# Kernel optimization log

Hardware: AMD Instinct MI355X
Metric: run time of the kernel (lower is better)

## Reference

```python
import jax, jax.numpy as jnp
import numpy as np

H = 512  # hidden_dim
IN = 4   # input_dim
OUT = 2  # output_dim
T_OBS = 30
T_PRED = 60
B = 4096


def _gru_cell(x, h, Wih, Whh, bih, bhh):
    # PyTorch GRU cell math. x: (B, D_in), h: (B, H)
    gi = x @ Wih.T + bih          # (B, 3H)
    gh = h @ Whh.T + bhh          # (B, 3H)
    i_r, i_z, i_n = jnp.split(gi, 3, axis=-1)
    h_r, h_z, h_n = jnp.split(gh, 3, axis=-1)
    r = jax.nn.sigmoid(i_r + h_r)
    z = jax.nn.sigmoid(i_z + h_z)
    n = jnp.tanh(i_n + r * h_n)
    return (1.0 - z) * n + z * h


def _gru_layer(xs, h0, Wih, Whh, bih, bhh):
    # xs: (T, B, D_in) -> outputs (T, B, H), final h (B, H)
    def step(h, x):
        h_new = _gru_cell(x, h, Wih, Whh, bih, bhh)
        return h_new, h_new
    h_last, ys = jax.lax.scan(step, h0, xs)
    return ys, h_last


def setup_inputs() -> dict:
    key = jax.random.key(0)
    ks = jax.random.split(key, 16)
    s = 0.05
    inp = {
        "x": jax.random.normal(ks[0], (B, T_OBS, IN), dtype=jnp.float32),
        # encoder layer 0
        "W_ih0": jax.random.normal(ks[1], (3 * H, IN)) * s,
        "W_hh0": jax.random.normal(ks[2], (3 * H, H)) * s,
        "b_ih0": jax.random.normal(ks[3], (3 * H,)) * s,
        "b_hh0": jax.random.normal(ks[4], (3 * H,)) * s,
        # encoder layer 1
        "W_ih1": jax.random.normal(ks[5], (3 * H, H)) * s,
        "W_hh1": jax.random.normal(ks[6], (3 * H, H)) * s,
        "b_ih1": jax.random.normal(ks[7], (3 * H,)) * s,
        "b_hh1": jax.random.normal(ks[8], (3 * H,)) * s,
        # decoder GRU (input_dim = OUT)
        "W_ihd": jax.random.normal(ks[9], (3 * H, OUT)) * s,
        "W_hhd": jax.random.normal(ks[10], (3 * H, H)) * s,
        "b_ihd": jax.random.normal(ks[11], (3 * H,)) * s,
        "b_hhd": jax.random.normal(ks[12], (3 * H,)) * s,
        # output head
        "W_fc": jax.random.normal(ks[13], (OUT, H)) * s,
        "b_fc": jax.random.normal(ks[14], (OUT,)) * s,
    }
    return inp


def reference(x, W_ih0, W_hh0, b_ih0, b_hh0, W_ih1, W_hh1, b_ih1, b_hh1,
              W_ihd, W_hhd, b_ihd, b_hhd, W_fc, b_fc):
    dtype = x.dtype
    xs = jnp.transpose(x, (1, 0, 2))  # (T, B, IN)
    h0 = jnp.zeros((x.shape[0], H), dtype=dtype)
    # 2-layer encoder GRU (dropout=identity at inference)
    ys0, _ = _gru_layer(xs, h0, W_ih0, W_hh0, b_ih0, b_hh0)
    ys1, h_last = _gru_layer(ys0, h0, W_ih1, W_hh1, b_ih1, b_hh1)
    dec_in0 = x[:, -1, :2]  # (B, 2)

    def dec_step(carry, _):
        h, inp = carry
        h_new = _gru_cell(inp, h, W_ihd, W_hhd, b_ihd, b_hhd)
        pred = h_new @ W_fc.T + b_fc  # (B, 2)
        return (h_new, pred), pred

    (_, _), preds = jax.lax.scan(dec_step, (h_last, dec_in0), None, length=T_PRED)
    return jnp.transpose(preds, (1, 0, 2))  # (B, T_PRED, OUT)
```

## Files before the change

kernel.cpp:

```cpp
#include <hip/hip_runtime.h>
#include <math.h>


#define B_SZ  4096
#define H     512
#define TOBS  30
#define TPRED 60

typedef float f32x4 __attribute__((ext_vector_type(4)));
typedef short s16x8 __attribute__((ext_vector_type(8)));
typedef __bf16 bf16x8 __attribute__((ext_vector_type(8)));

__device__ __forceinline__ float b2f(unsigned short u) {
    unsigned v = (unsigned)u << 16; return __builtin_bit_cast(float, v);
}
__device__ __forceinline__ unsigned short f2b(float f) {
    unsigned u = __builtin_bit_cast(unsigned, f);
    return (unsigned short)((u + 0x7FFF + ((u >> 16) & 1)) >> 16);
}

typedef __attribute__((address_space(1))) void gvoid;
typedef __attribute__((address_space(3))) void lvoid;
__device__ __forceinline__ void gl16(const void* g, void* l) {
    __builtin_amdgcn_global_load_lds((gvoid*)g, (lvoid*)l, 16, 0, 0);
}

__device__ __forceinline__ f32x4 mfma_bf16(s16x8 a, s16x8 b, f32x4 c) {
    return __builtin_amdgcn_mfma_f32_16x16x32_bf16(
        __builtin_bit_cast(bf16x8, a), __builtin_bit_cast(bf16x8, b), c, 0, 0, 0);
}

__device__ __forceinline__ float sigmoidf_(float v) { return 1.f / (1.f + expf(-v)); }

template<int NJ, int KTOT, int SPLIT>
__device__ __forceinline__ void gemm_core2(
    const unsigned short* __restrict__ A0, const unsigned short* __restrict__ A1,
    const unsigned short* __restrict__ W,
    int m0, int n0,
    unsigned short* __restrict__ sA, unsigned short* __restrict__ sB,
    f32x4 (&acc)[4][NJ + SPLIT])
{
    const int tid  = threadIdx.x;
    const int lane = tid & 63;
    const int w    = tid >> 6;
    const int wr = w >> 1, wc = w & 1;
    const int lr = lane & 15;
    const int q  = lane >> 4;
    const int wbase = tid & ~63;
    const int NT = KTOT / 64;
    const int ASZ = 128 * 64, BSZ = NJ * 32 * 64;

    auto stage = [&](int buf, int k0) {
        unsigned short* dA = sA + buf * ASZ;
        unsigned short* dB = sB + buf * BSZ;
        const unsigned short* Ab = (SPLIT && k0 >= 512) ? A1 : A0;
        const int ak0 = (SPLIT && k0 >= 512) ? k0 - 512 : k0;
#pragma unroll
        for (int s = 0; s < 4; ++s) {
            int i = s * 256 + tid;
            int row = i >> 3, p = i & 7;
            int c = p ^ (row & 7);
            gl16(Ab + (size_t)(m0 + row) * 512 + ak0 + c * 8, dA + (s * 256 + wbase) * 8);
        }
#pragma unroll
        for (int s = 0; s < NJ; ++s) {
            int i = s * 256 + tid;
            int row = i >> 3, p = i & 7;
            int c = p ^ (row & 7);
            gl16(W + (size_t)(n0 + row) * KTOT + k0 + c * 8, dB + (s * 256 + wbase) * 8);
        }
    };

    stage(0, 0);
    __syncthreads();
#pragma unroll
    for (int ti = 0; ti < NT; ++ti) {
        const int cur = ti & 1;
        if (ti + 1 < NT) stage(cur ^ 1, (ti + 1) * 64);
        const unsigned short* cA = sA + cur * ASZ;
        const unsigned short* cB = sB + cur * BSZ;
#pragma unroll
        for (int kk = 0; kk < 64; kk += 32) {
            int qb = (kk >> 3) + q;
            s16x8 af[4], bf[NJ];
#pragma unroll
            for (int fi = 0; fi < 4; ++fi) {
                int r = wr * 64 + fi * 16 + lr;
                af[fi] = *(const s16x8*)&cA[r * 64 + ((qb ^ (r & 7)) * 8)];
            }
#pragma unroll
            for (int fj = 0; fj < NJ; ++fj) {
                int r = wc * (NJ * 16) + fj * 16 + lr;
                bf[fj] = *(const s16x8*)&cB[r * 64 + ((qb ^ (r & 7)) * 8)];
            }
#pragma unroll
            for (int fi = 0; fi < 4; ++fi)
#pragma unroll
                for (int fj = 0; fj < NJ; ++fj) {
                    const int dst = (SPLIT && fj == NJ - 1 && ti >= NT / 2) ? NJ : fj;
                    acc[fi][dst] = mfma_bf16(af[fi], bf[fj], acc[fi][dst]);
                }
        }
        __syncthreads();
    }
}

__global__ __launch_bounds__(256)
void gemm_enc(const unsigned short* __restrict__ e1_h0, const unsigned short* __restrict__ e1_h1in,
              unsigned short* __restrict__ e1_h1out, const unsigned short* __restrict__ W1,
              const float* __restrict__ bih1, const float* __restrict__ bhh1,
              float* __restrict__ hf1,
              const unsigned short* __restrict__ e0_h0in, unsigned short* __restrict__ e0_h0out,
              const unsigned short* __restrict__ W0,
              const float* __restrict__ x, int t,
              const float* __restrict__ Wih0, const float* __restrict__ bih0,
              const float* __restrict__ bhh0, float* __restrict__ hf0,
              int roles)
{
    __shared__ unsigned short sA[2 * 128 * 64], sB[2 * 96 * 64];

    int bid = (int)blockIdx.x;
    bool isE1;
    if (roles == 3) { isE1 = bid < 512; bid &= 511; }
    else            { isE1 = (roles == 1); }

    int swz = (bid & 7) * 64 + (bid >> 3);
    const int tile_n = swz & 15;
    const int n0 = tile_n * 96;
    const int m0 = (swz >> 4) * 128;

    const int lane = threadIdx.x & 63;
    const int w    = threadIdx.x >> 6;
    const int wrw = w >> 1, wcw = w & 1;
    const int lr = lane & 15, q = lane >> 4;
    const int u = tile_n * 32 + wcw * 16 + lr;

    if (isE1) {
        f32x4 acc[4][4];
#pragma unroll
        for (int i = 0; i < 4; ++i)
#pragma unroll
            for (int j = 0; j < 4; ++j) acc[i][j] = (f32x4){0.f, 0.f, 0.f, 0.f};

        gemm_core2<3, 1024, 1>(e1_h0, e1_h1in, W1, m0, n0, sA, sB, acc);

        float br_ = bih1[u] + bhh1[u];
        float bz_ = bih1[512 + u] + bhh1[512 + u];
        float bni = bih1[1024 + u], bnh = bhh1[1024 + u];
#pragma unroll
        for (int fi = 0; fi < 4; ++fi) {
#pragma unroll
            for (int j = 0; j < 4; ++j) {
                int row = m0 + wrw * 64 + fi * 16 + q * 4 + j;
                float rr = sigmoidf_(acc[fi][0][j] + br_);
                float zz = sigmoidf_(acc[fi][1][j] + bz_);
                float nn = tanhf(acc[fi][2][j] + bni + rr * (acc[fi][3][j] + bnh));
                size_t hidx = (size_t)row * 512 + u;
                float hn = (1.f - zz) * nn + zz * hf1[hidx];
                hf1[hidx] = hn;
                e1_h1out[hidx] = f2b(hn);
            }
        }
    } else {
        f32x4 acc[4][3];
#pragma unroll
        for (int i = 0; i < 4; ++i)
#pragma unroll
            for (int j = 0; j < 3; ++j) acc[i][j] = (f32x4){0.f, 0.f, 0.f, 0.f};

        gemm_core2<3, 512, 0>(e0_h0in, e0_h0in, W0, m0, n0, sA, sB, acc);

        float4 wrv = *(const float4*)(Wih0 + (size_t)u * 4);
        float4 wzv = *(const float4*)(Wih0 + (size_t)(512 + u) * 4);
        float4 wnv = *(const float4*)(Wih0 + (size_t)(1024 + u) * 4);
        float br_ = bih0[u], bz_ = bih0[512 + u], bn_ = bih0[1024 + u];
        float cr_ = bhh0[u], cz_ = bhh0[512 + u], cn_ = bhh0[1024 + u];
#pragma unroll
        for (int fi = 0; fi < 4; ++fi) {
#pragma unroll
            for (int j = 0; j < 4; ++j) {
                int row = m0 + wrw * 64 + fi * 16 + q * 4 + j;
                float4 xv = *(const float4*)(x + (size_t)row * 120 + t * 4);
                float gir = br_ + xv.x * wrv.x + xv.y * wrv.y + xv.z * wrv.z + xv.w * wrv.w;
                float giz = bz_ + xv.x * wzv.x + xv.y * wzv.y + xv.z * wzv.z + xv.w * wzv.w;
                float gin = bn_ + xv.x * wnv.x + xv.y * wnv.y + xv.z * wnv.z + xv.w * wnv.w;
                float rr = sigmoidf_(gir + acc[fi][0][j] + cr_);
                float zz = sigmoidf_(giz + acc[fi][1][j] + cz_);
                float nn = tanhf(gin + rr * (acc[fi][2][j] + cn_));
                size_t hidx = (size_t)row * 512 + u;
                float hn = (1.f - zz) * nn + zz * hf0[hidx];
                hf0[hidx] = hn;
                e0_h0out[hidx] = f2b(hn);
            }
        }
    }
}

__global__ __launch_bounds__(256)
void gemm_d(const unsigned short* __restrict__ A ,
            const unsigned short* __restrict__ W,
            const float* __restrict__ dinbuf, int t,
            const float* __restrict__ Wih, const float* __restrict__ bih,
            const float* __restrict__ bhh, const float* __restrict__ bfc,
            float* __restrict__ hf, unsigned short* __restrict__ hbout,
            float* __restrict__ out)
{
    int bid = (int)blockIdx.x;
    int swz = (bid & 7) * 64 + (bid >> 3);
    const int tile_n = swz & 15;
    const int n0 = tile_n * 128;
    const int m0 = (swz >> 4) * 128;

    __shared__ unsigned short sA[2 * 128 * 64], sB[2 * 128 * 64];
    f32x4 acc[4][4];
#pragma unroll
    for (int i = 0; i < 4; ++i)
#pragma unroll
        for (int j = 0; j < 4; ++j) acc[i][j] = (f32x4){0.f, 0.f, 0.f, 0.f};

    gemm_core2<4, 512, 0>(A, A, W, m0, n0, sA, sB, acc);

    const int lane = threadIdx.x & 63;
    const int w    = threadIdx.x >> 6;
    const int wrw = w >> 1, wcw = w & 1;
    const int lr = lane & 15, q = lane >> 4;
    const int u = tile_n * 32 + wcw * 16 + lr;

    float wr0 = Wih[(size_t)u * 2],          wr1 = Wih[(size_t)u * 2 + 1];
    float wz0 = Wih[(size_t)(512 + u) * 2],  wz1 = Wih[(size_t)(512 + u) * 2 + 1];
    float wn0 = Wih[(size_t)(1024 + u) * 2], wn1 = Wih[(size_t)(1024 + u) * 2 + 1];
    float br_ = bih[u], bz_ = bih[512 + u], bn_ = bih[1024 + u];
    float cr_ = bhh[u], cz_ = bhh[512 + u], cn_ = bhh[1024 + u];
    float bfc0 = bfc[0], bfc1 = bfc[1];
    const bool wout = (tile_n == 0) && (wcw == 0) && (lr == 0);

#pragma unroll
    for (int fi = 0; fi < 4; ++fi) {
#pragma unroll
        for (int j = 0; j < 4; ++j) {
            int row = m0 + wrw * 64 + fi * 16 + q * 4 + j;
            float p0 = __shfl(acc[fi][3][j], (lane & 48) | 0) + bfc0;
            float p1 = __shfl(acc[fi][3][j], (lane & 48) | 1) + bfc1;
            float x0, x1;
            if (t == 0) { x0 = dinbuf[row * 2]; x1 = dinbuf[row * 2 + 1]; }
            else        { x0 = p0; x1 = p1; }
            float gir = br_ + x0 * wr0 + x1 * wr1;
            float giz = bz_ + x0 * wz0 + x1 * wz1;
            float gin = bn_ + x0 * wn0 + x1 * wn1;
            float rr = sigmoidf_(gir + acc[fi][0][j] + cr_);
            float zz = sigmoidf_(giz + acc[fi][1][j] + cz_);
            float nn = tanhf(gin + rr * (acc[fi][2][j] + cn_));
            size_t hidx = (size_t)row * 512 + u;
            float hn = (1.f - zz) * nn + zz * hf[hidx];
            hf[hidx] = hn;
            hbout[hidx] = f2b(hn);
            if (t > 0 && wout) {
                out[(size_t)row * 120 + (t - 1) * 2 + 0] = p0;
                out[(size_t)row * 120 + (t - 1) * 2 + 1] = p1;
            }
        }
    }
}

__global__ __launch_bounds__(64)
void fc_last(const unsigned short* __restrict__ hb, const float* __restrict__ Wfc,
             const float* __restrict__ bfc, float* __restrict__ out)
{
    int row = blockIdx.x, lane = threadIdx.x;
    const unsigned short* hrow = hb + (size_t)row * 512;
    float a0 = 0.f, a1 = 0.f;
#pragma unroll
    for (int kb = 0; kb < 8; ++kb) {
        int k = kb * 64 + lane;
        float hv = b2f(hrow[k]);
        a0 += hv * Wfc[k];
        a1 += hv * Wfc[512 + k];
    }
#pragma unroll
    for (int m = 32; m; m >>= 1) { a0 += __shfl_xor(a0, m); a1 += __shfl_xor(a1, m); }
    if (lane == 0) {
        out[(size_t)row * 120 + 118] = a0 + bfc[0];
        out[(size_t)row * 120 + 119] = a1 + bfc[1];
    }
}

__global__ void wprep_rzn(const float* __restrict__ s, unsigned short* __restrict__ d)
{
    int i = blockIdx.x * 256 + threadIdx.x;
    int c = i >> 9, k = i & 511;
    int ublock = c / 48, rem = c % 48, g = rem >> 4, uoff = rem & 15;
    int u = ublock * 16 + uoff;
    d[i] = f2b(s[((size_t)(g * 512 + u)) * 512 + k]);
}

__global__ void wprep_e1(const float* __restrict__ Wih1, const float* __restrict__ Whh1,
                         unsigned short* __restrict__ d)
{
    int i = blockIdx.x * 256 + threadIdx.x;
    int c = i >> 10, k = i & 1023;
    int ublock = c / 48, rem = c % 48, g = rem >> 4, uoff = rem & 15;
    int u = ublock * 16 + uoff;
    float v = (k < 512) ? Wih1[(size_t)(g * 512 + u) * 512 + k]
                        : Whh1[(size_t)(g * 512 + u) * 512 + (k - 512)];
    d[i] = f2b(v);
}

__global__ void wprep_d(const float* __restrict__ Whhd, const float* __restrict__ Wfc,
                        unsigned short* __restrict__ d)
{
    int i = blockIdx.x * 256 + threadIdx.x;
    int c = i >> 9, k = i & 511;
    int ublock = c >> 6, g = (c >> 4) & 3, uoff = c & 15;
    int u = ublock * 16 + uoff;
    float v;
    if (g < 3)           v = Whhd[((size_t)(g * 512 + u)) * 512 + k];
    else if (uoff < 2)   v = Wfc[(size_t)uoff * 512 + k];
    else                 v = 0.f;
    d[i] = f2b(v);
}

__global__ void init_all(const float* __restrict__ x,
                         float* __restrict__ hf0, float* __restrict__ hf1,
                         unsigned short* __restrict__ h0a, unsigned short* __restrict__ h1a,
                         float* __restrict__ dinbuf)
{
    int idx = blockIdx.x * 256 + threadIdx.x;
    hf0[idx] = 0.f; hf1[idx] = 0.f;
    h0a[idx] = 0; h1a[idx] = 0;
    if (idx < B_SZ * 2)
        dinbuf[idx] = x[(size_t)(idx >> 1) * 120 + 29 * 4 + (idx & 1)];
}

extern "C" void kernel_launch(void* const* d_in, const int* in_sizes, int n_in,
                              void* d_out, int out_size, void* d_ws, size_t ws_size,
                              hipStream_t stream)
{
    const float* x    = (const float*)d_in[0];
    const float* Wih0 = (const float*)d_in[1];
    const float* Whh0 = (const float*)d_in[2];
    const float* bih0 = (const float*)d_in[3];
    const float* bhh0 = (const float*)d_in[4];
    const float* Wih1 = (const float*)d_in[5];
    const float* Whh1 = (const float*)d_in[6];
    const float* bih1 = (const float*)d_in[7];
    const float* bhh1 = (const float*)d_in[8];
    const float* Wihd = (const float*)d_in[9];
    const float* Whhd = (const float*)d_in[10];
    const float* bihd = (const float*)d_in[11];
    const float* bhhd = (const float*)d_in[12];
    const float* Wfc  = (const float*)d_in[13];
    const float* bfc  = (const float*)d_in[14];
    float* out = (float*)d_out;

    char* p = (char*)d_ws;
    float* hf0 = (float*)p;  p += (size_t)B_SZ * 512 * 4;
    float* hf1 = (float*)p;  p += (size_t)B_SZ * 512 * 4;
    unsigned short* h0b_[2], *h1b_[2];
    h0b_[0] = (unsigned short*)p; p += (size_t)B_SZ * 512 * 2;
    h0b_[1] = (unsigned short*)p; p += (size_t)B_SZ * 512 * 2;
    h1b_[0] = (unsigned short*)p; p += (size_t)B_SZ * 512 * 2;
    h1b_[1] = (unsigned short*)p; p += (size_t)B_SZ * 512 * 2;
    float* dinbuf = (float*)p; p += (size_t)B_SZ * 2 * 4;
    unsigned short* W0p  = (unsigned short*)p; p += (size_t)1536 * 512 * 2;
    unsigned short* W1pp = (unsigned short*)p; p += (size_t)1536 * 1024 * 2;
    unsigned short* Wdp  = (unsigned short*)p;

    wprep_rzn<<<(1536 * 512) / 256, 256, 0, stream>>>(Whh0, W0p);
    wprep_e1<<<(1536 * 1024) / 256, 256, 0, stream>>>(Wih1, Whh1, W1pp);
    wprep_d<<<(2048 * 512) / 256, 256, 0, stream>>>(Whhd, Wfc, Wdp);
    init_all<<<(B_SZ * 512) / 256, 256, 0, stream>>>(x, hf0, hf1, h0b_[0], h1b_[0], dinbuf);

    gemm_enc<<<512, 256, 0, stream>>>(nullptr, nullptr, nullptr, nullptr, nullptr, nullptr,
                                      nullptr,
                                      h0b_[0], h0b_[1], W0p, x, 0, Wih0, bih0, bhh0, hf0,
                                      2);
    for (int t = 1; t < TOBS; ++t) {
        int s = t - 1;
        gemm_enc<<<1024, 256, 0, stream>>>(
            h0b_[(s + 1) & 1], h1b_[s & 1], h1b_[(s + 1) & 1], W1pp, bih1, bhh1, hf1,
            h0b_[t & 1], h0b_[(t + 1) & 1], W0p, x, t, Wih0, bih0, bhh0, hf0,
            3);
    }
    {
        int s = TOBS - 1;
        gemm_enc<<<512, 256, 0, stream>>>(
            h0b_[(s + 1) & 1], h1b_[s & 1], h1b_[(s + 1) & 1], W1pp, bih1, bhh1, hf1,
            nullptr, nullptr, nullptr, nullptr, 0, nullptr, nullptr, nullptr, nullptr,
            1);
    }
    for (int t = 0; t < TPRED; ++t) {
        gemm_d<<<512, 256, 0, stream>>>(h1b_[t & 1], Wdp, dinbuf, t, Wihd, bihd, bhhd, bfc,
                                        hf1, h1b_[(t + 1) & 1], out);
    }
    fc_last<<<B_SZ, 64, 0, stream>>>(h1b_[0], Wfc, bfc, out);
}
```

Baseline: 2.430 ms.

## Shrink GEMM K-tile to 32 and halve decoder M-tile for more blocks

The shared GEMM core now stages 32-wide K slices instead of 64, with a 4-way XOR swizzle in place of the 8-way one, and is parameterized on the number of M fragments. The decoder kernel switches to 64-row M tiles with a 1024-block grid, halving its per-block LDS and accumulator footprint. The intent is higher occupancy and more parallel blocks per launch to hide latency in these small per-timestep GEMMs. In exchange there are twice as many K iterations and __syncthreads per block, and the decoder's A reuse across N is lower.

```diff
diff --git a/kernel.cpp b/kernel.cpp
--- a/kernel.cpp
+++ b/kernel.cpp
@@ -32,13 +32,13 @@
 
 __device__ __forceinline__ float sigmoidf_(float v) { return 1.f / (1.f + expf(-v)); }
 
-template<int NJ, int KTOT, int SPLIT>
-__device__ __forceinline__ void gemm_core2(
+template<int MI, int NJ, int KTOT, int SPLIT>
+__device__ __forceinline__ void gemm_core32(
     const unsigned short* __restrict__ A0, const unsigned short* __restrict__ A1,
     const unsigned short* __restrict__ W,
     int m0, int n0,
     unsigned short* __restrict__ sA, unsigned short* __restrict__ sB,
-    f32x4 (&acc)[4][NJ + SPLIT])
+    f32x4 (&acc)[MI][NJ + SPLIT])
 {
     const int tid  = threadIdx.x;
     const int lane = tid & 63;
@@ -47,8 +47,10 @@
     const int lr = lane & 15;
     const int q  = lane >> 4;
     const int wbase = tid & ~63;
-    const int NT = KTOT / 64;
-    const int ASZ = 128 * 64, BSZ = NJ * 32 * 64;
+    const int NT  = KTOT / 32;
+    const int ASZ = MI * 1024, BSZ = NJ * 1024;
+    const int RA  = (MI * 128) / 256;
+    const int RB  = (NJ * 128 + 255) / 256;
 
     auto stage = [&](int buf, int k0) {
         unsigned short* dA = sA + buf * ASZ;
@@ -56,18 +58,20 @@
         const unsigned short* Ab = (SPLIT && k0 >= 512) ? A1 : A0;
         const int ak0 = (SPLIT && k0 >= 512) ? k0 - 512 : k0;
 #pragma unroll
-        for (int s = 0; s < 4; ++s) {
+        for (int s = 0; s < RA; ++s) {
             int i = s * 256 + tid;
-            int row = i >> 3, p = i & 7;
-            int c = p ^ (row & 7);
+            int row = i >> 2, p = i & 3;
+            int c = p ^ (row & 3);
             gl16(Ab + (size_t)(m0 + row) * 512 + ak0 + c * 8, dA + (s * 256 + wbase) * 8);
         }
 #pragma unroll
-        for (int s = 0; s < NJ; ++s) {
-            int i = s * 256 + tid;
-            int row = i >> 3, p = i & 7;
-            int c = p ^ (row & 7);
-            gl16(W + (size_t)(n0 + row) * KTOT + k0 + c * 8, dB + (s * 256 + wbase) * 8);
+        for (int s = 0; s < RB; ++s) {
+            if (s * 256 + wbase < NJ * 128) {
+                int i = s * 256 + tid;
+                int row = i >> 2, p = i & 3;
+                int c = p ^ (row & 3);
+                gl16(W + (size_t)(n0 + row) * KTOT + k0 + c * 8, dB + (s * 256 + wbase) * 8);
+            }
         }
     };
 
@@ -76,31 +80,27 @@
 #pragma unroll
     for (int ti = 0; ti < NT; ++ti) {
         const int cur = ti & 1;
-        if (ti + 1 < NT) stage(cur ^ 1, (ti + 1) * 64);
+        if (ti + 1 < NT) stage(cur ^ 1, (ti + 1) * 32);
         const unsigned short* cA = sA + cur * ASZ;
         const unsigned short* cB = sB + cur * BSZ;
-#pragma unroll
-        for (int kk = 0; kk < 64; kk += 32) {
-            int qb = (kk >> 3) + q;
-            s16x8 af[4], bf[NJ];
-#pragma unroll
-            for (int fi = 0; fi < 4; ++fi) {
-                int r = wr * 64 + fi * 16 + lr;
-                af[fi] = *(const s16x8*)&cA[r * 64 + ((qb ^ (r & 7)) * 8)];
-            }
+        s16x8 af[MI], bf[NJ];
+#pragma unroll
+        for (int fi = 0; fi < MI; ++fi) {
+            int r = wr * (MI * 16) + fi * 16 + lr;
+            af[fi] = *(const s16x8*)&cA[r * 32 + ((q ^ (r & 3)) * 8)];
+        }
+#pragma unroll
+        for (int fj = 0; fj < NJ; ++fj) {
+            int r = wc * (NJ * 16) + fj * 16 + lr;
+            bf[fj] = *(const s16x8*)&cB[r * 32 + ((q ^ (r & 3)) * 8)];
+        }
+#pragma unroll
+        for (int fi = 0; fi < MI; ++fi)
 #pragma unroll
             for (int fj = 0; fj < NJ; ++fj) {
-                int r = wc * (NJ * 16) + fj * 16 + lr;
-                bf[fj] = *(const s16x8*)&cB[r * 64 + ((qb ^ (r & 7)) * 8)];
-            }
-#pragma unroll
-            for (int fi = 0; fi < 4; ++fi)
-#pragma unroll
-                for (int fj = 0; fj < NJ; ++fj) {
-                    const int dst = (SPLIT && fj == NJ - 1 && ti >= NT / 2) ? NJ : fj;
-                    acc[fi][dst] = mfma_bf16(af[fi], bf[fj], acc[fi][dst]);
-                }
-        }
+                const int dst = (SPLIT && fj == NJ - 1 && ti >= NT / 2) ? NJ : fj;
+                acc[fi][dst] = mfma_bf16(af[fi], bf[fj], acc[fi][dst]);
+            }
         __syncthreads();
     }
 }
@@ -117,7 +117,7 @@
               const float* __restrict__ bhh0, float* __restrict__ hf0,
               int roles)
 {
-    __shared__ unsigned short sA[2 * 128 * 64], sB[2 * 96 * 64];
+    __shared__ unsigned short sA[2 * 128 * 32], sB[2 * 96 * 32];
 
     int bid = (int)blockIdx.x;
     bool isE1;
@@ -142,7 +142,7 @@
 #pragma unroll
             for (int j = 0; j < 4; ++j) acc[i][j] = (f32x4){0.f, 0.f, 0.f, 0.f};
 
-        gemm_core2<3, 1024, 1>(e1_h0, e1_h1in, W1, m0, n0, sA, sB, acc);
+        gemm_core32<4, 3, 1024, 1>(e1_h0, e1_h1in, W1, m0, n0, sA, sB, acc);
 
         float br_ = bih1[u] + bhh1[u];
         float bz_ = bih1[512 + u] + bhh1[512 + u];
@@ -168,7 +168,7 @@
 #pragma unroll
             for (int j = 0; j < 3; ++j) acc[i][j] = (f32x4){0.f, 0.f, 0.f, 0.f};
 
-        gemm_core2<3, 512, 0>(e0_h0in, e0_h0in, W0, m0, n0, sA, sB, acc);
+        gemm_core32<4, 3, 512, 0>(e0_h0in, e0_h0in, W0, m0, n0, sA, sB, acc);
 
         float4 wrv = *(const float4*)(Wih0 + (size_t)u * 4);
         float4 wzv = *(const float4*)(Wih0 + (size_t)(512 + u) * 4);
@@ -206,19 +206,19 @@
             float* __restrict__ out)
 {
     int bid = (int)blockIdx.x;
-    int swz = (bid & 7) * 64 + (bid >> 3);
+    int swz = (bid & 7) * 128 + (bid >> 3);
     const int tile_n = swz & 15;
     const int n0 = tile_n * 128;
-    const int m0 = (swz >> 4) * 128;
-
-    __shared__ unsigned short sA[2 * 128 * 64], sB[2 * 128 * 64];
-    f32x4 acc[4][4];
-#pragma unroll
-    for (int i = 0; i < 4; ++i)
+    const int m0 = (swz >> 4) * 64;
+
+    __shared__ unsigned short sA[2 * 64 * 32], sB[2 * 128 * 32];
+    f32x4 acc[2][4];
+#pragma unroll
+    for (int i = 0; i < 2; ++i)
 #pragma unroll
         for (int j = 0; j < 4; ++j) acc[i][j] = (f32x4){0.f, 0.f, 0.f, 0.f};
 
-    gemm_core2<4, 512, 0>(A, A, W, m0, n0, sA, sB, acc);
+    gemm_core32<2, 4, 512, 0>(A, A, W, m0, n0, sA, sB, acc);
 
     const int lane = threadIdx.x & 63;
     const int w    = threadIdx.x >> 6;
@@ -235,10 +235,10 @@
     const bool wout = (tile_n == 0) && (wcw == 0) && (lr == 0);
 
 #pragma unroll
-    for (int fi = 0; fi < 4; ++fi) {
+    for (int fi = 0; fi < 2; ++fi) {
 #pragma unroll
         for (int j = 0; j < 4; ++j) {
-            int row = m0 + wrw * 64 + fi * 16 + q * 4 + j;
+            int row = m0 + wrw * 32 + fi * 16 + q * 4 + j;
             float p0 = __shfl(acc[fi][3][j], (lane & 48) | 0) + bfc0;
             float p1 = __shfl(acc[fi][3][j], (lane & 48) | 1) + bfc1;
             float x0, x1;
@@ -389,8 +389,8 @@
             1);
     }
     for (int t = 0; t < TPRED; ++t) {
-        gemm_d<<<512, 256, 0, stream>>>(h1b_[t & 1], Wdp, dinbuf, t, Wihd, bihd, bhhd, bfc,
-                                        hf1, h1b_[(t + 1) & 1], out);
+        gemm_d<<<1024, 256, 0, stream>>>(h1b_[t & 1], Wdp, dinbuf, t, Wihd, bihd, bhhd, bfc,
+                                         hf1, h1b_[(t + 1) & 1], out);
     }
     fc_last<<<B_SZ, 64, 0, stream>>>(h1b_[0], Wfc, bfc, out);
 }
```

Result: no change. 2.446 ms (+0.7%).
